# Kernel optimization log

Measured on AMD Instinct MI355X. Metric: run time of the kernel, lower is better.

The kernel has to match this reference:

```python
import jax, jax.numpy as jnp
import numpy as np

B, D, K = 16384, 32, 128  # batch, cluster_dim, num_clusters


def setup_inputs() -> dict:
    key = jax.random.key(0)
    x = jax.random.normal(key, (B, D, K), dtype=jnp.float32)
    mu_0 = jnp.zeros((D, K), dtype=jnp.float32)                      # running mean buffer
    L_0 = jnp.broadcast_to(jnp.eye(D, dtype=jnp.float32), (K, D, D)) # running Cholesky buffer
    n_0 = jnp.ones((1,), dtype=jnp.float32)                          # running count
    return {"x": x, "mu_0": mu_0, "L_0": L_0, "n_0": n_0}


def reference(x, mu_0, L_0, n_0):
    # Training-mode forward of ClusterNorm1dv2.
    Bn = x.shape[0]
    eps_eye = jnp.eye(x.shape[1], dtype=x.dtype)
    n0 = n_0[0]
    x_mu = jnp.mean(x, axis=0)                         # [D, K]
    x_cnt = jnp.transpose(x - x_mu[None], (2, 1, 0))   # [K, D, B]
    C = jnp.einsum('kdb,keb->kde', x_cnt, x_cnt)       # [K, D, D] per-cluster scatter
    denom = n0 + Bn
    new_mu = (n0 * mu_0 + Bn * x_mu) / denom           # [D, K]
    x_d = jnp.transpose((x_mu - mu_0)[None], (2, 1, 0))  # [K, D, 1]
    new_cov = (jnp.einsum('kde,kfe->kdf', L_0, L_0) * (n0 / denom)
               + C / denom
               + jnp.einsum('kdo,keo->kde', x_d, x_d) * (n0 * Bn / denom ** 2))
    L = jnp.linalg.cholesky(new_cov + eps_eye)         # [K, D, D]
    xc = jnp.transpose(x - new_mu[None], (2, 1, 0))    # [K, D, B]
    Z = jax.scipy.linalg.solve_triangular(L, xc, lower=True)  # whitening solve
    return jnp.transpose(Z, (2, 1, 0))                 # [B, D, K]
```

## Files before the change

### kernel.cpp

```cpp
#include <hip/hip_runtime.h>

typedef __attribute__((ext_vector_type(4))) float f32x4;
typedef __attribute__((ext_vector_type(8))) short short8;

#define NB 16384
#define ND 32
#define NK 128

__device__ __forceinline__ unsigned bfbits(float f){
  union { float f; unsigned u; } v; v.f = f;
  const unsigned u = v.u;
  return (u + 0x7FFFu + ((u>>16)&1u)) >> 16;
}
__device__ __forceinline__ unsigned pkbf(float lo, float hi){
  return bfbits(lo) | (bfbits(hi) << 16);
}

__global__ __launch_bounds__(512, 2) void k1_scatter(const float* __restrict__ x,
                                                     float* __restrict__ part) {
  __shared__ float vs[16384];
  const int t = threadIdx.x;
  const int bx = blockIdx.x;
  const int ktile = bx & 3;
  const int cb = bx >> 2;
  const int k0 = ktile*32;

  const int shalf = t >> 8;
  const int d     = (t >> 3) & 31;
  const int kq    = t & 7;
  const float* xb = x + (size_t)d*128 + k0 + 4*kq;

  const int l = t & 63;
  const int w = t >> 6;

  f32x4 acc[4][4];
  f32x4 accS[4][2];
  #pragma unroll
  for (int c=0;c<4;c++){
    #pragma unroll
    for (int q=0;q<4;q++){ acc[c][q][0]=0.f; acc[c][q][1]=0.f; acc[c][q][2]=0.f; acc[c][q][3]=0.f; }
    #pragma unroll
    for (int q=0;q<2;q++){ accS[c][q][0]=0.f; accS[c][q][1]=0.f; accS[c][q][2]=0.f; accS[c][q][3]=0.f; }
  }

  const short8 ones = {0x3F80,0x3F80,0x3F80,0x3F80,0x3F80,0x3F80,0x3F80,0x3F80};
  unsigned* vsw = (unsigned*)vs;

  for (int ch = 0; ch < 8; ++ch) {
    const int sb = cb*256 + ch*32 + shalf*16;
    f32x4 La[8], Lb[8];
    #pragma unroll
    for (int p = 0; p < 8; ++p) {
      const int pr = (p + kq) & 7;
      const float* src = xb + (size_t)(sb + 2*pr)*4096;
      La[p] = *(const f32x4*)src;
      Lb[p] = *(const f32x4*)(src + 4096);
    }
    #pragma unroll
    for (int p = 0; p < 8; ++p) {
      const int pr = (p + kq) & 7;
      const int sp = shalf*8 + pr;
      #pragma unroll
      for (int i = 0; i < 4; ++i)
        vsw[(4*kq + i)*512 + d*16 + sp] = pkbf(La[p][i], Lb[p][i]);
    }
    __syncthreads();
    #pragma unroll
    for (int c = 0; c < 4; ++c) {
      const int kk = w*4 + c;
      const float* base = vs + kk*512;
      const short8 f0 = *(const short8*)(base + (l&15)*16      + (l>>4)*4);
      const short8 f1 = *(const short8*)(base + (l&15)*16 + 256 + (l>>4)*4);
      acc[c][0]  = __builtin_amdgcn_mfma_f32_16x16x32_bf16(f0, f0, acc[c][0], 0,0,0);
      acc[c][1]  = __builtin_amdgcn_mfma_f32_16x16x32_bf16(f0, f1, acc[c][1], 0,0,0);
      acc[c][2]  = __builtin_amdgcn_mfma_f32_16x16x32_bf16(f1, f0, acc[c][2], 0,0,0);
      acc[c][3]  = __builtin_amdgcn_mfma_f32_16x16x32_bf16(f1, f1, acc[c][3], 0,0,0);
      accS[c][0] = __builtin_amdgcn_mfma_f32_16x16x32_bf16(f0, ones, accS[c][0], 0,0,0);
      accS[c][1] = __builtin_amdgcn_mfma_f32_16x16x32_bf16(f1, ones, accS[c][1], 0,0,0);
    }
    __syncthreads();
  }

  const int col = l & 15, rw = (l >> 4) * 4;
  #pragma unroll
  for (int c = 0; c < 4; ++c) {
    const int kg = k0 + w*4 + c;
    float* pb = part + ((size_t)cb*128 + kg)*1056;
    #pragma unroll
    for (int i = 0; i < 2; ++i)
      #pragma unroll
      for (int j = 0; j < 2; ++j)
        #pragma unroll
        for (int r = 0; r < 4; ++r)
          pb[(i*16 + rw + r)*32 + j*16 + col] = acc[c][i*2+j][r];
    if (col == 0) {
      #pragma unroll
      for (int i = 0; i < 2; ++i)
        #pragma unroll
        for (int r = 0; r < 4; ++r)
          pb[1024 + i*16 + rw + r] = accS[c][i][r];
    }
  }
}

__global__ void k2a_reduce(const float* __restrict__ part, float* __restrict__ sfin) {
  const size_t idx = (size_t)blockIdx.x*256 + threadIdx.x;
  const float* p = part + idx;
  float a0=0.f,a1=0.f,a2=0.f,a3=0.f;
  for (int c = 0; c < 64; c += 4) {
    a0 += p[(size_t)(c+0)*135168];
    a1 += p[(size_t)(c+1)*135168];
    a2 += p[(size_t)(c+2)*135168];
    a3 += p[(size_t)(c+3)*135168];
  }
  sfin[idx] = (a0+a1)+(a2+a3);
}

__global__ void k2b_chol(const float* __restrict__ sfin,
                         const float* __restrict__ mu0,
                         const float* __restrict__ L0,
                         const float* __restrict__ n0p,
                         float* __restrict__ lpad,
                         float* __restrict__ nmu) {
  const int k = blockIdx.x;
  const int t = threadIdx.x;
  __shared__ float L0s[32*33];
  __shared__ float Am[32*33];
  __shared__ float xdl[32];
  __shared__ float dinv[32];
  const float n0 = n0p[0];
  const float denom = n0 + (float)NB;
  const float* sk = sfin + (size_t)k*1056;

  for (int idx = t; idx < 1024; idx += 256)
    L0s[(idx>>5)*33 + (idx&31)] = L0[k*1024 + idx];
  if (t < 32) {
    const float S  = sk[1024 + t];
    const float m0 = mu0[t*128 + k];
    nmu[t*128 + k] = (n0*m0 + S) / denom;
    xdl[t] = S*(1.0f/NB) - m0;
  }
  __syncthreads();

  const float c1 = n0/denom, c2 = 1.0f/denom;
  const float c3 = n0*(float)NB/(denom*denom);
  for (int idx = t; idx < 1024; idx += 256) {
    const int d = idx>>5, e = idx&31;
    const float M  = sk[d*32 + e];
    const float Sd = sk[1024 + d];
    const float Se = sk[1024 + e];
    const float C = M - Sd*Se*(1.0f/NB);
    float g = 0.f;
    #pragma unroll 8
    for (int f=0; f<32; f++) g += L0s[d*33+f]*L0s[e*33+f];
    float a = g*c1 + C*c2 + xdl[d]*xdl[e]*c3;
    if (d==e) a += 1.0f;
    Am[d*33+e] = a;
  }
  __syncthreads();

  for (int j=0;j<32;j++){
    float acc = 0.f;
    if (t < 32 && t >= j) {
      acc = Am[t*33+j];
      for (int e=0;e<j;e++) acc -= Am[t*33+e]*Am[j*33+e];
    }
    __syncthreads();
    if (t == j) {
      const float dj = sqrtf(acc);
      Am[j*33+j] = dj;
      dinv[j] = 1.0f/dj;
    }
    __syncthreads();
    if (t < 32 && t > j) Am[t*33+j] = acc*dinv[j];
    __syncthreads();
  }

  if (t < 32) {
    const int d = t;
    int rs = 0;
    for (int e=0;e<d;e++) rs += (e+3)>>2;
    rs *= 4;
    const int rl = ((d+3)>>2)*4;
    float* lp = lpad + k*576;
    for (int e=0;e<rl;e++) lp[rs+e] = (e<d) ? Am[d*33+e] : 0.f;
    lp[544+d] = dinv[d];
  }
}

__global__ __launch_bounds__(256, 2) void k3_whiten(const float* __restrict__ x,
                                                    const float* __restrict__ lpad,
                                                    const float* __restrict__ nmu,
                                                    float* __restrict__ out) {
  __shared__ float Lw[32*580];
  __shared__ float muL[32*32];
  const int t = threadIdx.x;
  const int bx = blockIdx.x;
  const int m = (bx >> 3) & 1;
  const int u = ((bx >> 4) << 3) | (bx & 7);
  const int ktile = ((u & 1) << 1) | m;
  const int chunk = u >> 1;
  const int k0 = ktile*32;

  {
    const f32x4* src = (const f32x4*)(lpad + (size_t)k0*576);
    #pragma unroll
    for (int q=0;q<18;q++){
      const int idx = t + q*256;
      const int row = idx/144, col = idx - row*144;
      *(f32x4*)(&Lw[row*580 + col*4]) = src[idx];
    }
    #pragma unroll
    for (int idx=t; idx<1024; idx+=256)
      muL[idx] = nmu[(idx>>5)*128 + k0 + (idx&31)];
  }
  __syncthreads();

  const int kl = t & 31;
  const int so = t >> 5;
  const float* Lrow = &Lw[kl*580];
  const int b0 = chunk*128;

  for (int it=0; it<4; ++it) {
    const int base = b0 + it*32 + so;
    const float* xa = x + (size_t)(base     )*4096 + k0 + kl;
    const float* xb = x + (size_t)(base +  8)*4096 + k0 + kl;
    const float* xc = x + (size_t)(base + 16)*4096 + k0 + kl;
    const float* xd = x + (size_t)(base + 24)*4096 + k0 + kl;
    float vA[32], vB[32], vC[32], vD[32];
    #pragma unroll
    for (int d=0; d<32; ++d) vA[d] = xa[d*128];
    #pragma unroll
    for (int d=0; d<32; ++d) vB[d] = xb[d*128];
    #pragma unroll
    for (int d=0; d<32; ++d) vC[d] = xc[d*128];
    #pragma unroll
    for (int d=0; d<32; ++d) vD[d] = xd[d*128];
    #pragma unroll
    for (int d=0; d<32; ++d) {
      const float m2 = muL[d*32 + kl];
      vA[d] -= m2; vB[d] -= m2; vC[d] -= m2; vD[d] -= m2;
    }
    int rs = 0;
    #pragma unroll
    for (int d=0; d<32; ++d) {
      float sA = vA[d], sB = vB[d], sC = vC[d], sD = vD[d];
      const int nq = (d+3)>>2;
      #pragma unroll
      for (int q=0; q<nq; ++q) {
        const f32x4 Lq = *(const f32x4*)(Lrow + rs + 4*q);
        sA -= Lq[0]*vA[4*q+0] + Lq[1]*vA[4*q+1] + Lq[2]*vA[4*q+2] + Lq[3]*vA[4*q+3];
        sB -= Lq[0]*vB[4*q+0] + Lq[1]*vB[4*q+1] + Lq[2]*vB[4*q+2] + Lq[3]*vB[4*q+3];
        sC -= Lq[0]*vC[4*q+0] + Lq[1]*vC[4*q+1] + Lq[2]*vC[4*q+2] + Lq[3]*vC[4*q+3];
        sD -= Lq[0]*vD[4*q+0] + Lq[1]*vD[4*q+1] + Lq[2]*vD[4*q+2] + Lq[3]*vD[4*q+3];
      }
      const float di = Lrow[544+d];
      vA[d] = sA*di; vB[d] = sB*di; vC[d] = sC*di; vD[d] = sD*di;
      rs += 4*nq;
    }
    float* oa = out + (size_t)(base     )*4096 + k0 + kl;
    float* ob = out + (size_t)(base +  8)*4096 + k0 + kl;
    float* oc = out + (size_t)(base + 16)*4096 + k0 + kl;
    float* od = out + (size_t)(base + 24)*4096 + k0 + kl;
    #pragma unroll
    for (int d=0; d<32; ++d) __builtin_nontemporal_store(vA[d], oa + d*128);
    #pragma unroll
    for (int d=0; d<32; ++d) __builtin_nontemporal_store(vB[d], ob + d*128);
    #pragma unroll
    for (int d=0; d<32; ++d) __builtin_nontemporal_store(vC[d], oc + d*128);
    #pragma unroll
    for (int d=0; d<32; ++d) __builtin_nontemporal_store(vD[d], od + d*128);
  }
}

extern "C" void kernel_launch(void* const* d_in, const int* in_sizes, int n_in,
                              void* d_out, int out_size, void* d_ws, size_t ws_size,
                              hipStream_t stream) {
  const float* x   = (const float*)d_in[0];
  const float* mu0 = (const float*)d_in[1];
  const float* L0  = (const float*)d_in[2];
  const float* n0  = (const float*)d_in[3];
  float* out  = (float*)d_out;
  float* part = out;
  float* sfin = out + 8650752;
  float* lpad = (float*)d_ws;
  float* nmu  = lpad + 128*576;

  k1_scatter<<<256, 512, 0, stream>>>(x, part);
  k2a_reduce<<<528, 256, 0, stream>>>(part, sfin);
  k2b_chol  <<<128, 256, 0, stream>>>(sfin, mu0, L0, n0, lpad, nmu);
  k3_whiten <<<512, 256, 0, stream>>>(x, lpad, nmu, out);
}
```

Measured before the change: 198.7 us.

## Prefetch next chunk into registers, swizzle LDS slots, compute column sums in FP32

Software-pipelines the scatter kernel so that the global loads for the next chunk are issued right after the LDS store barrier and overlap with the MFMA phase. It replaces the staggered load order with an XOR-style slot swizzle on both the LDS writes and the fragment reads, to avoid bank conflicts. The per-column sums, previously computed by extra MFMAs against a ones vector, are now accumulated in FP32 registers and reduced through a small shared buffer. This cuts MFMA work and raises sum precision, but adds register pressure from holding two chunks' loads and extra shared memory.

Result: slower. 205.0 us (+3.1%).

```diff
diff --git a/kernel.cpp b/kernel.cpp
--- a/kernel.cpp
+++ b/kernel.cpp
@@ -19,6 +19,7 @@
 __global__ __launch_bounds__(512, 2) void k1_scatter(const float* __restrict__ x,
                                                      float* __restrict__ part) {
   __shared__ float vs[16384];
+  __shared__ float ssr[2048];
   const int t = threadIdx.x;
   const int bx = blockIdx.x;
   const int ktile = bx & 3;
@@ -34,49 +35,58 @@
   const int w = t >> 6;
 
   f32x4 acc[4][4];
-  f32x4 accS[4][2];
   #pragma unroll
-  for (int c=0;c<4;c++){
+  for (int c=0;c<4;c++)
     #pragma unroll
     for (int q=0;q<4;q++){ acc[c][q][0]=0.f; acc[c][q][1]=0.f; acc[c][q][2]=0.f; acc[c][q][3]=0.f; }
-    #pragma unroll
-    for (int q=0;q<2;q++){ accS[c][q][0]=0.f; accS[c][q][1]=0.f; accS[c][q][2]=0.f; accS[c][q][3]=0.f; }
-  }
-
-  const short8 ones = {0x3F80,0x3F80,0x3F80,0x3F80,0x3F80,0x3F80,0x3F80,0x3F80};
+  float ssum[4] = {0.f,0.f,0.f,0.f};
+
   unsigned* vsw = (unsigned*)vs;
-
-  for (int ch = 0; ch < 8; ++ch) {
-    const int sb = cb*256 + ch*32 + shalf*16;
-    f32x4 La[8], Lb[8];
+  f32x4 La[8], Lb[8];
+
+  {
+    const int sb = cb*256 + shalf*16;
     #pragma unroll
     for (int p = 0; p < 8; ++p) {
-      const int pr = (p + kq) & 7;
-      const float* src = xb + (size_t)(sb + 2*pr)*4096;
+      const float* src = xb + (size_t)(sb + 2*p)*4096;
       La[p] = *(const f32x4*)src;
       Lb[p] = *(const f32x4*)(src + 4096);
     }
+  }
+
+  #pragma unroll
+  for (int ch = 0; ch < 8; ++ch) {
     #pragma unroll
     for (int p = 0; p < 8; ++p) {
-      const int pr = (p + kq) & 7;
-      const int sp = shalf*8 + pr;
+      const int sp = shalf*8 + p;
       #pragma unroll
-      for (int i = 0; i < 4; ++i)
-        vsw[(4*kq + i)*512 + d*16 + sp] = pkbf(La[p][i], Lb[p][i]);
-    }
-    __syncthreads();
+      for (int i = 0; i < 4; ++i) {
+        const int slot = (sp + 4*((kq + i) & 3)) & 15;
+        vsw[(4*kq + i)*512 + d*16 + slot] = pkbf(La[p][i], Lb[p][i]);
+        ssum[i] += La[p][i] + Lb[p][i];
+      }
+    }
+    __syncthreads();
+    if (ch < 7) {
+      const int sb = cb*256 + (ch+1)*32 + shalf*16;
+      #pragma unroll
+      for (int p = 0; p < 8; ++p) {
+        const float* src = xb + (size_t)(sb + 2*p)*4096;
+        La[p] = *(const f32x4*)src;
+        Lb[p] = *(const f32x4*)(src + 4096);
+      }
+    }
     #pragma unroll
     for (int c = 0; c < 4; ++c) {
       const int kk = w*4 + c;
       const float* base = vs + kk*512;
-      const short8 f0 = *(const short8*)(base + (l&15)*16      + (l>>4)*4);
-      const short8 f1 = *(const short8*)(base + (l&15)*16 + 256 + (l>>4)*4);
-      acc[c][0]  = __builtin_amdgcn_mfma_f32_16x16x32_bf16(f0, f0, acc[c][0], 0,0,0);
-      acc[c][1]  = __builtin_amdgcn_mfma_f32_16x16x32_bf16(f0, f1, acc[c][1], 0,0,0);
-      acc[c][2]  = __builtin_amdgcn_mfma_f32_16x16x32_bf16(f1, f0, acc[c][2], 0,0,0);
-      acc[c][3]  = __builtin_amdgcn_mfma_f32_16x16x32_bf16(f1, f1, acc[c][3], 0,0,0);
-      accS[c][0] = __builtin_amdgcn_mfma_f32_16x16x32_bf16(f0, ones, accS[c][0], 0,0,0);
-      accS[c][1] = __builtin_amdgcn_mfma_f32_16x16x32_bf16(f1, ones, accS[c][1], 0,0,0);
+      const int sg = 4*(((l>>4) + w + c) & 3);
+      const short8 f0 = *(const short8*)(base + (l&15)*16       + sg);
+      const short8 f1 = *(const short8*)(base + (l&15)*16 + 256 + sg);
+      acc[c][0] = __builtin_amdgcn_mfma_f32_16x16x32_bf16(f0, f0, acc[c][0], 0,0,0);
+      acc[c][1] = __builtin_amdgcn_mfma_f32_16x16x32_bf16(f0, f1, acc[c][1], 0,0,0);
+      acc[c][2] = __builtin_amdgcn_mfma_f32_16x16x32_bf16(f1, f0, acc[c][2], 0,0,0);
+      acc[c][3] = __builtin_amdgcn_mfma_f32_16x16x32_bf16(f1, f1, acc[c][3], 0,0,0);
     }
     __syncthreads();
   }
@@ -93,13 +103,14 @@
         #pragma unroll
         for (int r = 0; r < 4; ++r)
           pb[(i*16 + rw + r)*32 + j*16 + col] = acc[c][i*2+j][r];
-    if (col == 0) {
-      #pragma unroll
-      for (int i = 0; i < 2; ++i)
-        #pragma unroll
-        for (int r = 0; r < 4; ++r)
-          pb[1024 + i*16 + rw + r] = accS[c][i][r];
-    }
+  }
+  #pragma unroll
+  for (int i = 0; i < 4; ++i)
+    ssr[shalf*1024 + d*32 + 4*kq + i] = ssum[i];
+  __syncthreads();
+  for (int ii = t; ii < 1024; ii += 512) {
+    const int dd = ii >> 5, kk2 = ii & 31;
+    part[((size_t)cb*128 + k0 + kk2)*1056 + 1024 + dd] = ssr[ii] + ssr[1024 + ii];
   }
 }
 
```
